# Optimization experiments

Hardware: AMD Instinct MI355X
Metric: run time of the kernel (lower is better)

Reference implementation:

```python
import jax, jax.numpy as jnp
from jax import lax
import numpy as np

OUT_H, OUT_W = 8, 32
SCALE = 4.0
B, CIN, COUT, H, W = 4, 256, 128, 256, 256
N_PER_IMG = 32
N_ROIS = B * N_PER_IMG


def setup_inputs() -> dict:
    key = jax.random.key(0)
    k = jax.random.split(key, 6)
    feats = jax.random.normal(k[0], (B, CIN, H, W), jnp.float32)
    rng = np.random.default_rng(0)
    # rois sorted by batch index so output ordering matches the torch double loop
    bidx = np.repeat(np.arange(B), N_PER_IMG).astype(np.float32)
    x1 = rng.uniform(0, W * SCALE * 0.6, N_ROIS)
    y1 = rng.uniform(0, H * SCALE * 0.6, N_ROIS)
    bw = rng.uniform(48, W * SCALE * 0.35, N_ROIS)
    bh = rng.uniform(32, H * SCALE * 0.25, N_ROIS)
    rois = jnp.asarray(np.stack([bidx, x1, y1, x1 + bw, y1 + bh], 1), jnp.float32)
    # rescaled per-ROI bitmap masks at feature resolution (values 0/1)
    masks = (jax.random.uniform(k[1], (N_ROIS, H, W)) > 0.5).astype(jnp.float32)
    conv_w = jax.random.normal(k[2], (COUT, CIN, 3, 3), jnp.float32) * 0.02
    conv_b = jnp.zeros((COUT,), jnp.float32)
    bn_gamma = jnp.ones((COUT,), jnp.float32)
    bn_beta = jnp.zeros((COUT,), jnp.float32)
    bn_mean = jax.random.normal(k[3], (COUT,), jnp.float32) * 0.1
    bn_var = jax.random.uniform(k[4], (COUT,), jnp.float32, 0.5, 1.5)
    return dict(feats=feats, rois=rois, masks=masks, conv_w=conv_w, conv_b=conv_b,
                bn_gamma=bn_gamma, bn_beta=bn_beta, bn_mean=bn_mean, bn_var=bn_var)


def _forward(feats, rois, masks, conv_w, conv_b, bn_gamma, bn_beta, bn_mean, bn_var):
    # conv3x3(pad=1) + BN(eval) + ReLU
    feat = lax.conv_general_dilated(feats, conv_w, (1, 1), 'SAME',
                                    dimension_numbers=('NCHW', 'OIHW', 'NCHW'))
    feat = feat + conv_b[None, :, None, None]
    scale = (bn_gamma / jnp.sqrt(bn_var + 1e-5))[None, :, None, None]
    feat = (feat - bn_mean[None, :, None, None]) * scale + bn_beta[None, :, None, None]
    feat = jax.nn.relu(feat)
    Hf, Wf = feat.shape[2], feat.shape[3]

    pad = jnp.array([-1.0, -1.0, 1.0, 1.0], jnp.float32)
    # torch .long() truncates toward zero; astype(int32) matches for these values
    boxes = (rois[:, 1:] / SCALE + pad).astype(jnp.int32)
    l = jnp.clip(boxes[:, 0], 0, Wf)
    t = jnp.clip(boxes[:, 1], 0, Hf)
    r = jnp.clip(boxes[:, 2], 0, Wf)
    b = jnp.clip(boxes[:, 3], 0, Hf)
    bi = rois[:, 0].astype(jnp.int32)

    ii = jnp.arange(OUT_H, dtype=jnp.float32) + 0.5
    jj = jnp.arange(OUT_W, dtype=jnp.float32) + 0.5

    def one_roi(bi_r, l_r, t_r, r_r, b_r, mask_r):
        ch = (b_r - t_r).astype(jnp.float32)
        cw = (r_r - l_r).astype(jnp.float32)
        transpose = ch > 1.5 * cw  # tall crops get transposed before resize
        ones_row = jnp.ones((1, OUT_W), jnp.float32)
        ones_col = jnp.ones((OUT_H, 1), jnp.float32)
        # source coords (align_corners=False): (dst+0.5)*src/dst_size - 0.5
        V = jnp.where(transpose,
                      (jj * ch / OUT_W - 0.5)[None, :] * ones_col,
                      (ii * ch / OUT_H - 0.5)[:, None] * ones_row)
        U = jnp.where(transpose,
                      (ii * cw / OUT_H - 0.5)[:, None] * ones_row,
                      (jj * cw / OUT_W - 0.5)[None, :] * ones_col)
        V = jnp.maximum(V, 0.0)
        U = jnp.maximum(U, 0.0)
        chi = jnp.maximum(b_r - t_r, 1)
        cwi = jnp.maximum(r_r - l_r, 1)
        vf = jnp.floor(V)
        uf = jnp.floor(U)
        y0 = jnp.minimum(vf.astype(jnp.int32), chi - 1)
        y1 = jnp.minimum(y0 + 1, chi - 1)
        x0 = jnp.minimum(uf.astype(jnp.int32), cwi - 1)
        x1 = jnp.minimum(x0 + 1, cwi - 1)
        wy = V - vf
        wx = U - uf
        ay0 = jnp.clip(t_r + y0, 0, Hf - 1)
        ay1 = jnp.clip(t_r + y1, 0, Hf - 1)
        ax0 = jnp.clip(l_r + x0, 0, Wf - 1)
        ax1 = jnp.clip(l_r + x1, 0, Wf - 1)

        def samp(ay, ax):
            v = feat[bi_r, :, ay, ax]  # (OUT_H, OUT_W, C) gather
            return jnp.moveaxis(v, -1, 0) * mask_r[ay, ax][None]  # (C, OUT_H, OUT_W)

        out = (((1 - wy) * (1 - wx))[None] * samp(ay0, ax0)
               + ((1 - wy) * wx)[None] * samp(ay0, ax1)
               + (wy * (1 - wx))[None] * samp(ay1, ax0)
               + (wy * wx)[None] * samp(ay1, ax1))
        valid = jnp.logical_and(r_r > l_r, b_r > t_r)
        return jnp.where(valid, out, 0.0)

    return jax.vmap(one_roi)(bi, l, t, r, b, masks)  # (N, C, OUT_H, OUT_W)


def reference(feats, rois, masks, conv_w, conv_b, bn_gamma, bn_beta, bn_mean, bn_var):
    return _forward(feats, rois, masks, conv_w, conv_b, bn_gamma, bn_beta, bn_mean, bn_var)
```

## Files before the change

kernel.cpp:

```cpp
#include <hip/hip_runtime.h>

typedef __attribute__((ext_vector_type(8))) short short8;
typedef __attribute__((ext_vector_type(4))) float float4v;

static __device__ __forceinline__ unsigned short f2bf(float x) {
    unsigned u = __float_as_uint(x);
    return (unsigned short)((u + 0x7fffu + ((u >> 16) & 1u)) >> 16);
}
static __device__ __forceinline__ int imin(int a, int b) { return a < b ? a : b; }
static __device__ __forceinline__ int imax(int a, int b) { return a > b ? a : b; }

static __device__ __forceinline__ void gload_lds16(const void* g, void* l) {
    __builtin_amdgcn_global_load_lds(
        (const __attribute__((address_space(1))) void*)g,
        (__attribute__((address_space(3))) void*)l, 16, 0, 0);
}

__global__ void wprep_kernel(const float* __restrict__ conv_w,
                             unsigned short* __restrict__ wprep,
                             unsigned short* __restrict__ zguard) {
    if (blockIdx.x == 0 && threadIdx.x < 32) zguard[threadIdx.x] = 0;
    int e = blockIdx.x * 256 + threadIdx.x;
    if (e >= 294912) return;
    int ci = e & 31;
    int t2 = e >> 5;
    int co = t2 & 127;
    int t3 = t2 >> 7;
    int tap = t3 % 9;
    int chunk = t3 / 9;
    int cin = chunk * 32 + ci;
    int ty = tap / 3, tx = tap - ty * 3;
    wprep[e] = f2bf(conv_w[((co * 256 + cin) * 3 + ty) * 3 + tx]);
}

__global__ __launch_bounds__(256) void prep_kernel(const float* __restrict__ feats_b,
                                                   unsigned short* __restrict__ fb16) {
    const int bx = blockIdx.x;
    const int chunk = bx >> 8;
    const int h = bx & 255;
    const int w = threadIdx.x;
    const float* src = feats_b + ((size_t)(chunk * 32) * 256 + h) * 256 + w;
    union { unsigned short u16[32]; short8 v8[4]; } p;
#pragma unroll
    for (int ci = 0; ci < 32; ++ci)
        p.u16[ci] = f2bf(src[(size_t)ci * 65536]);
    unsigned short* dst = fb16 + ((size_t)(chunk * 256 + h) * 256 + w) * 32;
#pragma unroll
    for (int k = 0; k < 4; ++k)
        *(short8*)(dst + k * 8) = p.v8[k];
}

__global__ __launch_bounds__(256, 2) void conv_bn_relu_kernel(
    const unsigned short* __restrict__ fb16,
    const float* __restrict__ conv_b,
    const float* __restrict__ bn_gamma,
    const float* __restrict__ bn_beta,
    const float* __restrict__ bn_mean,
    const float* __restrict__ bn_var,
    const unsigned short* __restrict__ wprep,
    const unsigned short* __restrict__ zguard,
    unsigned short* __restrict__ feat_cl_b) {

    __shared__ __align__(16) unsigned short in_lds[6 * 34 * 32];
    __shared__ float aL[128], bL[128];

    const int tid = threadIdx.x;
    const int rem = blockIdx.x;
    const int h0  = (rem >> 3) * 4;
    const int w0  = (rem & 7) * 32;

    if (tid < 128) {
        float s = bn_gamma[tid] * rsqrtf(bn_var[tid] + 1e-5f);
        aL[tid] = s;
        bL[tid] = (conv_b[tid] - bn_mean[tid]) * s + bn_beta[tid];
    }

    const int wave = tid >> 6;
    const int lane = tid & 63;
    const int q    = lane >> 4;
    const int l15  = lane & 15;

    long off_s[4];
    int  lds_s[4];
    bool oob_s[4];
#pragma unroll
    for (int i = 0; i < 4; ++i) {
        int u = wave * 204 + i * 64 + lane;
        int row = u / 136;
        int r2  = u - row * 136;
        int col = r2 >> 2;
        int part = r2 & 3;
        int gh = h0 - 1 + row;
        int gw = w0 - 1 + col;
        oob_s[i] = ((unsigned)gh > 255u) || ((unsigned)gw > 255u);
        off_s[i] = (long)(gh * 256 + gw) * 32 + part * 8;
        lds_s[i] = u * 8;
    }

    float4v acc[2][8];
#pragma unroll
    for (int a = 0; a < 2; ++a)
#pragma unroll
        for (int p = 0; p < 8; ++p)
            acc[a][p] = (float4v){0.f, 0.f, 0.f, 0.f};

    for (int chunk = 0; chunk < 8; ++chunk) {
        const unsigned short* fb = fb16 + (size_t)chunk * (65536u * 32u);
#pragma unroll
        for (int i = 0; i < 3; ++i) {
            const unsigned short* gp = oob_s[i] ? zguard : (fb + off_s[i]);
            gload_lds16(gp, &in_lds[lds_s[i]]);
        }
        if (lane < 12) {
            const unsigned short* gp = oob_s[3] ? zguard : (fb + off_s[3]);
            gload_lds16(gp, &in_lds[lds_s[3]]);
        }
        __syncthreads();

#pragma unroll
        for (int tap = 0; tap < 9; ++tap) {
            const int dy = tap / 3, dx = tap - dy * 3;
            const short8* wpt = (const short8*)wprep + (chunk * 9 + tap) * 512;
            short8 a0 = wpt[(wave * 32 + l15) * 4 + q];
            short8 a1 = wpt[(wave * 32 + 16 + l15) * 4 + q];
#pragma unroll
            for (int pt = 0; pt < 8; ++pt) {
                const int r  = pt >> 1;
                const int c0 = (pt & 1) * 16;
                short8 bf = *(const short8*)&in_lds[((r + dy) * 34 + (c0 + l15 + dx)) * 32 + q * 8];
                acc[0][pt] = __builtin_amdgcn_mfma_f32_16x16x32_bf16(a0, bf, acc[0][pt], 0, 0, 0);
                acc[1][pt] = __builtin_amdgcn_mfma_f32_16x16x32_bf16(a1, bf, acc[1][pt], 0, 0, 0);
            }
        }
        __syncthreads();
    }

#pragma unroll
    for (int ct = 0; ct < 2; ++ct) {
        const int coutb = wave * 32 + ct * 16 + q * 4;
        const float s0 = aL[coutb + 0], s1 = aL[coutb + 1];
        const float s2 = aL[coutb + 2], s3 = aL[coutb + 3];
        const float o0 = bL[coutb + 0], o1 = bL[coutb + 1];
        const float o2 = bL[coutb + 2], o3 = bL[coutb + 3];
#pragma unroll
        for (int pt = 0; pt < 8; ++pt) {
            const int r  = pt >> 1;
            const int cl = (pt & 1) * 16 + l15;
            float4v v = acc[ct][pt];
            unsigned short p0 = f2bf(fmaxf(v[0] * s0 + o0, 0.f));
            unsigned short p1 = f2bf(fmaxf(v[1] * s1 + o1, 0.f));
            unsigned short p2 = f2bf(fmaxf(v[2] * s2 + o2, 0.f));
            unsigned short p3 = f2bf(fmaxf(v[3] * s3 + o3, 0.f));
            unsigned long long pk = (unsigned long long)p0
                                  | ((unsigned long long)p1 << 16)
                                  | ((unsigned long long)p2 << 32)
                                  | ((unsigned long long)p3 << 48);
            size_t off = ((size_t)((h0 + r) * 256 + (w0 + cl))) * 128 + coutb;
            *(unsigned long long*)(feat_cl_b + off) = pk;
        }
    }
}

__global__ __launch_bounds__(256) void roi_gather_kernel(
    const float* __restrict__ rois,
    const float* __restrict__ masks,
    const unsigned long long* __restrict__ feat_u64,
    float* __restrict__ out) {

    __shared__ int   offs[64][4];
    __shared__ float wts[64][4];

    const int blk = blockIdx.x;
    const int roi = blk >> 2;
    const int q0  = blk & 3;
    const int tid = threadIdx.x;

    const float* rp = rois + roi * 5;
    const int bi = (int)rp[0];
    int l_ = (int)(rp[1] * 0.25f - 1.0f);
    int t_ = (int)(rp[2] * 0.25f - 1.0f);
    int r_ = (int)(rp[3] * 0.25f + 1.0f);
    int b_ = (int)(rp[4] * 0.25f + 1.0f);
    l_ = imin(imax(l_, 0), 256); t_ = imin(imax(t_, 0), 256);
    r_ = imin(imax(r_, 0), 256); b_ = imin(imax(b_, 0), 256);
    const float ch = (float)(b_ - t_);
    const float cw = (float)(r_ - l_);
    const bool transpose = ch > 1.5f * cw;
    const int chi = imax(b_ - t_, 1);
    const int cwi = imax(r_ - l_, 1);
    const float vscale = ((r_ > l_) && (b_ > t_)) ? 1.f : 0.f;

    {
        const int pos_l  = tid >> 2;
        const int corner = tid & 3;
        const int pos = q0 * 64 + pos_l;
        const int i = pos >> 5, j = pos & 31;
        const float fi = (float)i + 0.5f, fj = (float)j + 0.5f;
        float V = transpose ? (fj * ch * (1.f / 32.f) - 0.5f)
                            : (fi * ch * (1.f / 8.f)  - 0.5f);
        float U = transpose ? (fi * cw * (1.f / 8.f)  - 0.5f)
                            : (fj * cw * (1.f / 32.f) - 0.5f);
        V = fmaxf(V, 0.f); U = fmaxf(U, 0.f);
        float vf = floorf(V), uf = floorf(U);
        int y0 = imin((int)vf, chi - 1); int y1 = imin(y0 + 1, chi - 1);
        int x0 = imin((int)uf, cwi - 1); int x1 = imin(x0 + 1, cwi - 1);
        float wy = V - vf, wx = U - uf;
        int ay = imin(imax(t_ + ((corner & 2) ? y1 : y0), 0), 255);
        int ax = imin(imax(l_ + ((corner & 1) ? x1 : x0), 0), 255);
        float wgt = ((corner & 2) ? wy : (1.f - wy)) * ((corner & 1) ? wx : (1.f - wx));
        wts[pos_l][corner]  = wgt * masks[(size_t)roi * 65536 + ay * 256 + ax] * vscale;
        offs[pos_l][corner] = (ay * 256 + ax) * 32;
    }
    __syncthreads();

    const int cq = tid & 31;
    const int pq = tid >> 5;
    const unsigned long long* fb = feat_u64 + (size_t)bi * (65536ull * 32ull) + cq;
    float* op = out + (size_t)roi * 32768 + (size_t)cq * 4 * 256 + q0 * 64;

#pragma unroll 2
    for (int po = 0; po < 8; ++po) {
        const int pos_l = po * 8 + pq;
        float a0 = 0.f, a1 = 0.f, a2 = 0.f, a3 = 0.f;
#pragma unroll
        for (int k = 0; k < 4; ++k) {
            unsigned long long u = fb[offs[pos_l][k]];
            float w = wts[pos_l][k];
            a0 += w * __uint_as_float((unsigned)(u)       << 16);
            a1 += w * __uint_as_float((unsigned)(u >> 16) << 16);
            a2 += w * __uint_as_float((unsigned)(u >> 32) << 16);
            a3 += w * __uint_as_float((unsigned)(u >> 48) << 16);
        }
        op[pos_l]       = a0;
        op[pos_l + 256] = a1;
        op[pos_l + 512] = a2;
        op[pos_l + 768] = a3;
    }
}

extern "C" void kernel_launch(void* const* d_in, const int* in_sizes, int n_in,
                              void* d_out, int out_size, void* d_ws, size_t ws_size,
                              hipStream_t stream) {
    const float* feats    = (const float*)d_in[0];
    const float* rois     = (const float*)d_in[1];
    const float* masks    = (const float*)d_in[2];
    const float* conv_w   = (const float*)d_in[3];
    const float* conv_b   = (const float*)d_in[4];
    const float* bn_gamma = (const float*)d_in[5];
    const float* bn_beta  = (const float*)d_in[6];
    const float* bn_mean  = (const float*)d_in[7];
    const float* bn_var   = (const float*)d_in[8];
    float* out = (float*)d_out;

    unsigned short* wprep   = (unsigned short*)d_ws;
    unsigned short* zguard  = (unsigned short*)((char*)d_ws + 0x90000);
    unsigned short* feat_cl = (unsigned short*)((char*)d_ws + (1ull << 20));
    unsigned short* fb16    = (unsigned short*)((char*)d_ws + (1ull << 20) + (64ull << 20));

    hipLaunchKernelGGL(wprep_kernel, dim3(1152), dim3(256), 0, stream,
                       conv_w, wprep, zguard);
    for (int b = 0; b < 4; ++b) {
        hipLaunchKernelGGL(prep_kernel, dim3(2048), dim3(256), 0, stream,
                           feats + (size_t)b * 256 * 65536, fb16);
        hipLaunchKernelGGL(conv_bn_relu_kernel, dim3(512), dim3(256), 0, stream,
                           fb16, conv_b, bn_gamma, bn_beta, bn_mean, bn_var,
                           wprep, zguard, feat_cl + (size_t)b * 65536 * 128);
    }
    hipLaunchKernelGGL(roi_gather_kernel, dim3(512), dim3(256), 0, stream,
                       rois, masks, (const unsigned long long*)feat_cl, out);
}
```

Before: 582.7 us.

## Batch all images in one conv launch with larger tiles and double-buffered LDS

The per-image loop of prep and conv launches is replaced by single launches covering all four images, using a 4x64 pixel tile per block. Each wave now computes 64 output channels by 32 pixels, which gives more reuse of loaded weights and input fragments. The input halo is double-buffered in LDS so the next channel chunk's global-to-LDS copy overlaps the MFMA work on the current chunk, and one barrier per chunk is dropped. The cost is double the accumulator registers and larger LDS use, which may lower occupancy. The fb16 workspace now has to hold all four images at once.

```diff
diff --git a/kernel.cpp b/kernel.cpp
--- a/kernel.cpp
+++ b/kernel.cpp
@@ -33,18 +33,20 @@
     wprep[e] = f2bf(conv_w[((co * 256 + cin) * 3 + ty) * 3 + tx]);
 }
 
-__global__ __launch_bounds__(256) void prep_kernel(const float* __restrict__ feats_b,
+__global__ __launch_bounds__(256) void prep_kernel(const float* __restrict__ feats,
                                                    unsigned short* __restrict__ fb16) {
     const int bx = blockIdx.x;
-    const int chunk = bx >> 8;
+    const int b = bx >> 11;
+    const int chunk = (bx >> 8) & 7;
     const int h = bx & 255;
     const int w = threadIdx.x;
-    const float* src = feats_b + ((size_t)(chunk * 32) * 256 + h) * 256 + w;
+    const float* src = feats + (((size_t)b * 256 + chunk * 32) * 256 + h) * 256 + w;
     union { unsigned short u16[32]; short8 v8[4]; } p;
 #pragma unroll
     for (int ci = 0; ci < 32; ++ci)
         p.u16[ci] = f2bf(src[(size_t)ci * 65536]);
-    unsigned short* dst = fb16 + ((size_t)(chunk * 256 + h) * 256 + w) * 32;
+    unsigned short* dst = fb16 + (size_t)b * 16777216
+                        + ((size_t)(chunk * 256 + h) * 256 + w) * 32;
 #pragma unroll
     for (int k = 0; k < 4; ++k)
         *(short8*)(dst + k * 8) = p.v8[k];
@@ -59,15 +61,17 @@
     const float* __restrict__ bn_var,
     const unsigned short* __restrict__ wprep,
     const unsigned short* __restrict__ zguard,
-    unsigned short* __restrict__ feat_cl_b) {
-
-    __shared__ __align__(16) unsigned short in_lds[6 * 34 * 32];
+    unsigned short* __restrict__ feat_cl) {
+
+    __shared__ __align__(16) unsigned short in_lds[2][12672];
     __shared__ float aL[128], bL[128];
 
     const int tid = threadIdx.x;
-    const int rem = blockIdx.x;
-    const int h0  = (rem >> 3) * 4;
-    const int w0  = (rem & 7) * 32;
+    const int bx  = blockIdx.x;
+    const int b   = bx >> 8;
+    const int rem = bx & 255;
+    const int h0  = (rem >> 2) * 4;
+    const int w0  = (rem & 3) * 64;
 
     if (tid < 128) {
         float s = bn_gamma[tid] * rsqrtf(bn_var[tid] + 1e-5f);
@@ -75,21 +79,23 @@
         bL[tid] = (conv_b[tid] - bn_mean[tid]) * s + bn_beta[tid];
     }
 
-    const int wave = tid >> 6;
-    const int lane = tid & 63;
-    const int q    = lane >> 4;
-    const int l15  = lane & 15;
-
-    long off_s[4];
-    int  lds_s[4];
-    bool oob_s[4];
-#pragma unroll
-    for (int i = 0; i < 4; ++i) {
-        int u = wave * 204 + i * 64 + lane;
-        int row = u / 136;
-        int r2  = u - row * 136;
-        int col = r2 >> 2;
-        int part = r2 & 3;
+    const int wave   = tid >> 6;
+    const int lane   = tid & 63;
+    const int q      = lane >> 4;
+    const int l15    = lane & 15;
+    const int cohalf = wave >> 1;
+    const int phalf  = wave & 1;
+
+    long off_s[7];
+    int  lds_s[7];
+    bool oob_s[7];
+#pragma unroll
+    for (int i = 0; i < 7; ++i) {
+        int u = (i < 6) ? (i * 256 + tid) : (1536 + tid);
+        int pix = u >> 2;
+        int part = u & 3;
+        int row = pix / 66;
+        int col = pix - row * 66;
         int gh = h0 - 1 + row;
         int gw = w0 - 1 + col;
         oob_s[i] = ((unsigned)gh > 255u) || ((unsigned)gw > 255u);
@@ -97,55 +103,72 @@
         lds_s[i] = u * 8;
     }
 
-    float4v acc[2][8];
-#pragma unroll
-    for (int a = 0; a < 2; ++a)
+    const unsigned short* fbb = fb16 + (size_t)b * 16777216;
+
+    float4v acc[4][8];
+#pragma unroll
+    for (int a = 0; a < 4; ++a)
 #pragma unroll
         for (int p = 0; p < 8; ++p)
             acc[a][p] = (float4v){0.f, 0.f, 0.f, 0.f};
 
+    {
+        const unsigned short* fb = fbb;
+#pragma unroll
+        for (int i = 0; i < 6; ++i)
+            gload_lds16(oob_s[i] ? zguard : (fb + off_s[i]), &in_lds[0][lds_s[i]]);
+        if (tid < 48)
+            gload_lds16(oob_s[6] ? zguard : (fb + off_s[6]), &in_lds[0][lds_s[6]]);
+    }
+    __syncthreads();
+
     for (int chunk = 0; chunk < 8; ++chunk) {
-        const unsigned short* fb = fb16 + (size_t)chunk * (65536u * 32u);
-#pragma unroll
-        for (int i = 0; i < 3; ++i) {
-            const unsigned short* gp = oob_s[i] ? zguard : (fb + off_s[i]);
-            gload_lds16(gp, &in_lds[lds_s[i]]);
-        }
-        if (lane < 12) {
-            const unsigned short* gp = oob_s[3] ? zguard : (fb + off_s[3]);
-            gload_lds16(gp, &in_lds[lds_s[3]]);
-        }
-        __syncthreads();
-
+        if (chunk < 7) {
+            const unsigned short* fb = fbb + (size_t)(chunk + 1) * 2097152;
+            unsigned short* lb = in_lds[(chunk + 1) & 1];
+#pragma unroll
+            for (int i = 0; i < 6; ++i)
+                gload_lds16(oob_s[i] ? zguard : (fb + off_s[i]), &lb[lds_s[i]]);
+            if (tid < 48)
+                gload_lds16(oob_s[6] ? zguard : (fb + off_s[6]), &lb[lds_s[6]]);
+        }
+
+        const unsigned short* lb = in_lds[chunk & 1];
 #pragma unroll
         for (int tap = 0; tap < 9; ++tap) {
             const int dy = tap / 3, dx = tap - dy * 3;
-            const short8* wpt = (const short8*)wprep + (chunk * 9 + tap) * 512;
-            short8 a0 = wpt[(wave * 32 + l15) * 4 + q];
-            short8 a1 = wpt[(wave * 32 + 16 + l15) * 4 + q];
+            const short8* wpt = (const short8*)wprep
+                              + ((chunk * 9 + tap) * 128 + cohalf * 64) * 4;
+            short8 a0 = wpt[(l15     ) * 4 + q];
+            short8 a1 = wpt[(l15 + 16) * 4 + q];
+            short8 a2 = wpt[(l15 + 32) * 4 + q];
+            short8 a3 = wpt[(l15 + 48) * 4 + q];
 #pragma unroll
             for (int pt = 0; pt < 8; ++pt) {
                 const int r  = pt >> 1;
-                const int c0 = (pt & 1) * 16;
-                short8 bf = *(const short8*)&in_lds[((r + dy) * 34 + (c0 + l15 + dx)) * 32 + q * 8];
+                const int cc = phalf * 32 + (pt & 1) * 16 + l15 + dx;
+                short8 bf = *(const short8*)&lb[((r + dy) * 66 + cc) * 32 + q * 8];
                 acc[0][pt] = __builtin_amdgcn_mfma_f32_16x16x32_bf16(a0, bf, acc[0][pt], 0, 0, 0);
                 acc[1][pt] = __builtin_amdgcn_mfma_f32_16x16x32_bf16(a1, bf, acc[1][pt], 0, 0, 0);
+                acc[2][pt] = __builtin_amdgcn_mfma_f32_16x16x32_bf16(a2, bf, acc[2][pt], 0, 0, 0);
+                acc[3][pt] = __builtin_amdgcn_mfma_f32_16x16x32_bf16(a3, bf, acc[3][pt], 0, 0, 0);
             }
         }
-        __syncthreads();
-    }
-
-#pragma unroll
-    for (int ct = 0; ct < 2; ++ct) {
-        const int coutb = wave * 32 + ct * 16 + q * 4;
-        const float s0 = aL[coutb + 0], s1 = aL[coutb + 1];
-        const float s2 = aL[coutb + 2], s3 = aL[coutb + 3];
-        const float o0 = bL[coutb + 0], o1 = bL[coutb + 1];
-        const float o2 = bL[coutb + 2], o3 = bL[coutb + 3];
+        if (chunk < 7) __syncthreads();
+    }
+
+    unsigned short* fcb = feat_cl + (size_t)b * 8388608;
+#pragma unroll
+    for (int ct = 0; ct < 4; ++ct) {
+        const int co = cohalf * 64 + ct * 16 + q * 4;
+        const float s0 = aL[co + 0], s1 = aL[co + 1];
+        const float s2 = aL[co + 2], s3 = aL[co + 3];
+        const float o0 = bL[co + 0], o1 = bL[co + 1];
+        const float o2 = bL[co + 2], o3 = bL[co + 3];
 #pragma unroll
         for (int pt = 0; pt < 8; ++pt) {
             const int r  = pt >> 1;
-            const int cl = (pt & 1) * 16 + l15;
+            const int cl = w0 + phalf * 32 + (pt & 1) * 16 + l15;
             float4v v = acc[ct][pt];
             unsigned short p0 = f2bf(fmaxf(v[0] * s0 + o0, 0.f));
             unsigned short p1 = f2bf(fmaxf(v[1] * s1 + o1, 0.f));
@@ -155,8 +178,8 @@
                                   | ((unsigned long long)p1 << 16)
                                   | ((unsigned long long)p2 << 32)
                                   | ((unsigned long long)p3 << 48);
-            size_t off = ((size_t)((h0 + r) * 256 + (w0 + cl))) * 128 + coutb;
-            *(unsigned long long*)(feat_cl_b + off) = pk;
+            size_t off = ((size_t)((h0 + r) * 256 + cl)) * 128 + co;
+            *(unsigned long long*)(fcb + off) = pk;
         }
     }
 }
@@ -255,17 +278,14 @@
     unsigned short* wprep   = (unsigned short*)d_ws;
     unsigned short* zguard  = (unsigned short*)((char*)d_ws + 0x90000);
     unsigned short* feat_cl = (unsigned short*)((char*)d_ws + (1ull << 20));
-    unsigned short* fb16    = (unsigned short*)((char*)d_ws + (1ull << 20) + (64ull << 20));
+    unsigned short* fb16    = (unsigned short*)((char*)d_ws + (65ull << 20));
 
     hipLaunchKernelGGL(wprep_kernel, dim3(1152), dim3(256), 0, stream,
                        conv_w, wprep, zguard);
-    for (int b = 0; b < 4; ++b) {
-        hipLaunchKernelGGL(prep_kernel, dim3(2048), dim3(256), 0, stream,
-                           feats + (size_t)b * 256 * 65536, fb16);
-        hipLaunchKernelGGL(conv_bn_relu_kernel, dim3(512), dim3(256), 0, stream,
-                           fb16, conv_b, bn_gamma, bn_beta, bn_mean, bn_var,
-                           wprep, zguard, feat_cl + (size_t)b * 65536 * 128);
-    }
+    hipLaunchKernelGGL(prep_kernel, dim3(8192), dim3(256), 0, stream, feats, fb16);
+    hipLaunchKernelGGL(conv_bn_relu_kernel, dim3(1024), dim3(256), 0, stream,
+                       fb16, conv_b, bn_gamma, bn_beta, bn_mean, bn_var,
+                       wprep, zguard, feat_cl);
     hipLaunchKernelGGL(roi_gather_kernel, dim3(512), dim3(256), 0, stream,
                        rois, masks, (const unsigned long long*)feat_cl, out);
 }
```

Result: slower. 638.9 us (+9.6%).
